# Optimization experiments

Hardware: AMD Instinct MI355X
Metric: run time of the kernel (lower is better)

Reference implementation:

```python
import jax, jax.numpy as jnp
import numpy as np

B, L, S, D, H = 32, 256, 64, 128, 4
DH = D // H
EPS = 1e-5


def _uniform(k, shape, scale):
    return jax.random.uniform(k, shape, jnp.float32, -scale, scale)


def setup_inputs() -> dict:
    key = jax.random.key(0)
    ks = jax.random.split(key, 12)
    sc = 1.0 / np.sqrt(D)
    return {
        "h_wq": jax.random.normal(ks[0], (B, L, D), jnp.float32),
        "h_all": jax.random.normal(ks[1], (B, L, S, D), jnp.float32),
        "station_id": jax.random.randint(ks[2], (B,), 0, S),
        "adj": jax.random.randint(ks[3], (S, S), 0, 2).astype(jnp.float32),
        "in_proj_w": _uniform(ks[4], (3 * D, D), sc),
        "in_proj_b": _uniform(ks[5], (3 * D,), sc),
        "out_w": _uniform(ks[6], (D, D), sc),
        "out_b": _uniform(ks[7], (D,), sc),
        "gate_w": _uniform(ks[8], (D, 2 * D), 1.0 / np.sqrt(2 * D)),
        "gate_b": _uniform(ks[9], (D,), 1.0 / np.sqrt(2 * D)),
        "ln_g": jnp.ones((D,), jnp.float32),
        "ln_b": jnp.zeros((D,), jnp.float32),
        "alpha": jnp.asarray(0.1, jnp.float32),
    }


def _allowed_mask(adj, station_id):
    # allowed[b, s] == True  <=> station s may attend as key for sample b
    sid = station_id.astype(jnp.int32)
    allowed = adj[sid] > 0.0                                  # [B, S]
    self_oh = jax.nn.one_hot(sid, adj.shape[0], dtype=bool)   # [B, S]
    allowed = allowed & ~self_oh                              # exclude self
    # fallback-to-all for rows with no neighbor (still excluding self)
    no_nb = ~jnp.any(allowed, axis=1, keepdims=True)
    allowed = jnp.where(no_nb, ~self_oh, allowed)
    # final safety: if STILL empty (S==1 edge case), allow self
    no_nb2 = ~jnp.any(allowed, axis=1, keepdims=True)
    allowed = allowed | (no_nb2 & self_oh)
    return allowed


def _forward(h_wq, h_all, station_id, adj, in_proj_w, in_proj_b,
             out_w, out_b, gate_w, gate_b, ln_g, ln_b, alpha):
    b, l, d = h_wq.shape
    s = h_all.shape[2]
    qw, kw, vw = jnp.split(in_proj_w, 3, axis=0)
    qb, kb, vb = jnp.split(in_proj_b, 3, axis=0)

    q = (h_wq @ qw.T + qb).reshape(b, l, H, DH)        # [B,L,H,DH]
    k = (h_all @ kw.T + kb).reshape(b, l, s, H, DH)    # [B,L,S,H,DH]
    v = (h_all @ vw.T + vb).reshape(b, l, s, H, DH)

    scores = jnp.einsum('blhd,blshd->blhs', q, k) / np.sqrt(DH)  # [B,L,H,S]
    allowed = _allowed_mask(adj, station_id)                     # [B,S]
    scores = jnp.where(allowed[:, None, None, :], scores, -jnp.inf)
    w = jax.nn.softmax(scores, axis=-1)

    ctx = jnp.einsum('blhs,blshd->blhd', w, v).reshape(b, l, d)
    ctx = ctx @ out_w.T + out_b                                  # out_proj

    g = jax.nn.sigmoid(jnp.concatenate([h_wq, ctx], axis=-1) @ gate_w.T + gate_b)
    y = h_wq + alpha * (g * ctx)                                 # dropout = eval mode

    mu = jnp.mean(y, axis=-1, keepdims=True)
    var = jnp.mean(jnp.square(y - mu), axis=-1, keepdims=True)
    return (y - mu) * jax.lax.rsqrt(var + EPS) * ln_g + ln_b


def reference(h_wq, h_all, station_id, adj, in_proj_w, in_proj_b,
              out_w, out_b, gate_w, gate_b, ln_g, ln_b, alpha):
    return _forward(h_wq, h_all, station_id, adj, in_proj_w, in_proj_b,
                    out_w, out_b, gate_w, gate_b, ln_g, ln_b, alpha)
```

## Files before the change

kernel.cpp:

```cpp
#include <hip/hip_runtime.h>
#include <math.h>

#define B_   32
#define L_   256
#define S_   64
#define D_   128
#define H_   4
#define DH_  32
#define NTOK (B_*L_)

#define QK_OFF   0
#define QK_BYTES ((size_t)NTOK*512*4)
#define CB_OFF   (QK_OFF + QK_BYTES)
#define CB_BYTES ((size_t)NTOK*4*4)
#define CTX_OFF  (CB_OFF + CB_BYTES)

__global__ __launch_bounds__(256) void qk_kernel(
        const float* __restrict__ h_wq,
        const float* __restrict__ in_proj_w, const float* __restrict__ in_proj_b,
        float* __restrict__ qk_out, float* __restrict__ cb_out) {
    __shared__ float x_lds[32*128];
    __shared__ float q_lds[32*128];
    const int t0 = blockIdx.x * 32;
    const int tid = threadIdx.x;

    {
        const float4* src = (const float4*)(h_wq + (size_t)t0*128);
        float4* dst = (float4*)x_lds;
        for (int e = tid; e < 32*32; e += 256) dst[e] = src[e];
    }
    __syncthreads();

    const int d = tid & 127, half = tid >> 7;
    const float* xb = x_lds + half*16*128;
    {
        float acc[16];
        const float qb = in_proj_b[d];
        #pragma unroll
        for (int t = 0; t < 16; ++t) acc[t] = qb;
        const float4* wrow = (const float4*)(in_proj_w + (size_t)d*128);
        for (int j4 = 0; j4 < 32; ++j4) {
            float4 w = wrow[j4];
            #pragma unroll
            for (int t = 0; t < 16; ++t) {
                float4 x = *(const float4*)(xb + t*128 + j4*4);
                acc[t] += w.x*x.x + w.y*x.y + w.z*x.z + w.w*x.w;
            }
        }
        #pragma unroll
        for (int t = 0; t < 16; ++t) q_lds[(half*16+t)*128 + d] = acc[t];
    }
    __syncthreads();

    const float scale = 0.17677669529663687f;
    const float* qbse = q_lds + half*16*128;
    #pragma unroll
    for (int h = 0; h < 4; ++h) {
        float acc[16];
        #pragma unroll
        for (int t = 0; t < 16; ++t) acc[t] = 0.f;
        for (int j = 0; j < 32; ++j) {
            float w = in_proj_w[(size_t)(128 + h*32 + j)*128 + d];
            #pragma unroll
            for (int t = 0; t < 16; ++t) acc[t] += w * qbse[t*128 + h*32 + j];
        }
        #pragma unroll
        for (int t = 0; t < 16; ++t)
            qk_out[(size_t)(t0 + half*16 + t)*512 + h*128 + d] = acc[t] * scale;
    }
    if (tid < 128) {
        int t = tid >> 2, h = tid & 3;
        float s = 0.f;
        for (int j = 0; j < 32; ++j)
            s += q_lds[t*128 + h*32 + j] * in_proj_b[128 + h*32 + j];
        cb_out[(t0 + t)*4 + h] = s * scale;
    }
}

__global__ __launch_bounds__(256) void attn_kernel(
        const float* __restrict__ h_all,
        const float* __restrict__ in_proj_w, const float* __restrict__ in_proj_b,
        const float* __restrict__ qk_buf, const float* __restrict__ cb_buf,
        const int* __restrict__ station_id, const float* __restrict__ adj,
        float* __restrict__ ctx_out) {
    __shared__ float qk_lds[4][4*132];
    __shared__ float sc[4][4*64];
    __shared__ float u_lds[4][4*132];
    __shared__ int   lst[64];
    __shared__ int   cnt_s;
    __shared__ float cb[4][4];

    const int t0  = blockIdx.x * 4;
    const int b   = t0 >> 8;
    const int tid = threadIdx.x;
    const int wv  = tid >> 6;
    const int lane = tid & 63;
    const int t = t0 + wv;

    if (tid < 64) {
        int sid = station_id[b];
        int s = tid;
        bool av = (adj[sid*S_ + s] > 0.0f) && (s != sid);
        unsigned long long m = __ballot(av);
        if (m == 0ull) { av = (s != sid); m = __ballot(av); }
        if (m == 0ull) { av = (s == sid); m = __ballot(av); }
        int idx = __popcll(m & ((1ull << s) - 1ull));
        if (av) lst[idx] = s;
        if (s == 0) cnt_s = __popcll(m);
    }

    {
        const float4* src = (const float4*)(qk_buf + (size_t)t*512);
        for (int e = lane; e < 128; e += 64) {
            int h = e >> 5, d4 = e & 31;
            *(float4*)&qk_lds[wv][h*132 + d4*4] = src[e];
        }
    }
    if (lane < 4) cb[wv][lane] = cb_buf[t*4 + lane];
    __syncthreads();

    const int cnt = cnt_s;
    const float* rowbase = h_all + (size_t)t * (S_*D_);

    for (int p = lane; p < 4*cnt; p += 64) {
        int h = p & 3, i = p >> 2;
        float acc = cb[wv][h];
        const float4* qr = (const float4*)(&qk_lds[wv][h*132]);
        const float4* rr = (const float4*)(rowbase + lst[i]*D_);
        #pragma unroll 8
        for (int j = 0; j < 32; ++j) {
            float4 a = qr[j], x = rr[j];
            acc += a.x*x.x + a.y*x.y + a.z*x.z + a.w*x.w;
        }
        sc[wv][h*64 + i] = acc;
    }

    {
        int j = lane & 31;
        for (int h = (lane >> 5); h < 4; h += 2) {
            float v0 = (j < cnt)      ? sc[wv][h*64 + j]      : -INFINITY;
            float v1 = (j + 32 < cnt) ? sc[wv][h*64 + j + 32] : -INFINITY;
            float m = fmaxf(v0, v1);
            for (int o = 16; o >= 1; o >>= 1) m = fmaxf(m, __shfl_xor(m, o, 32));
            float e0 = (j < cnt)      ? __expf(v0 - m) : 0.f;
            float e1 = (j + 32 < cnt) ? __expf(v1 - m) : 0.f;
            float ssum = e0 + e1;
            for (int o = 16; o >= 1; o >>= 1) ssum += __shfl_xor(ssum, o, 32);
            float inv = 1.0f / ssum;
            sc[wv][h*64 + j]      = e0 * inv;
            sc[wv][h*64 + j + 32] = e1 * inv;
        }
    }

    {
        float2 u0 = {0.f,0.f}, u1 = {0.f,0.f}, u2 = {0.f,0.f}, u3 = {0.f,0.f};
        #pragma unroll 4
        for (int i = 0; i < cnt; ++i) {
            float2 x = *(const float2*)(rowbase + lst[i]*D_ + 2*lane);
            float w0 = sc[wv][i], w1 = sc[wv][64+i], w2 = sc[wv][128+i], w3 = sc[wv][192+i];
            u0.x += w0*x.x; u0.y += w0*x.y;
            u1.x += w1*x.x; u1.y += w1*x.y;
            u2.x += w2*x.x; u2.y += w2*x.y;
            u3.x += w3*x.x; u3.y += w3*x.y;
        }
        *(float2*)&u_lds[wv][0*132 + 2*lane] = u0;
        *(float2*)&u_lds[wv][1*132 + 2*lane] = u1;
        *(float2*)&u_lds[wv][2*132 + 2*lane] = u2;
        *(float2*)&u_lds[wv][3*132 + 2*lane] = u3;
    }
    __syncthreads();

    if (tid < 128) {
        const int d = tid, h = d >> 5;
        const float4* vwrow = (const float4*)(in_proj_w + (size_t)(256 + d)*128);
        const float vb = in_proj_b[256 + d];
        float a0 = vb, a1 = vb, a2 = vb, a3 = vb;
        #pragma unroll 8
        for (int j4 = 0; j4 < 32; ++j4) {
            float4 w = vwrow[j4];
            float4 u0 = *(const float4*)(&u_lds[0][h*132 + j4*4]);
            float4 u1 = *(const float4*)(&u_lds[1][h*132 + j4*4]);
            float4 u2 = *(const float4*)(&u_lds[2][h*132 + j4*4]);
            float4 u3 = *(const float4*)(&u_lds[3][h*132 + j4*4]);
            a0 += w.x*u0.x + w.y*u0.y + w.z*u0.z + w.w*u0.w;
            a1 += w.x*u1.x + w.y*u1.y + w.z*u1.z + w.w*u1.w;
            a2 += w.x*u2.x + w.y*u2.y + w.z*u2.z + w.w*u2.w;
            a3 += w.x*u3.x + w.y*u3.y + w.z*u3.z + w.w*u3.w;
        }
        ctx_out[(size_t)(t0+0)*128 + d] = a0;
        ctx_out[(size_t)(t0+1)*128 + d] = a1;
        ctx_out[(size_t)(t0+2)*128 + d] = a2;
        ctx_out[(size_t)(t0+3)*128 + d] = a3;
    }
}

__global__ __launch_bounds__(256) void epi_kernel(
        const float* __restrict__ h_wq, const float* __restrict__ ctx_buf,
        const float* __restrict__ out_w, const float* __restrict__ out_b,
        const float* __restrict__ gate_w, const float* __restrict__ gate_b,
        const float* __restrict__ ln_g, const float* __restrict__ ln_b,
        const float* __restrict__ alpha, float* __restrict__ out) {
    __shared__ float c_tile[32*128];
    __shared__ float x_tile[32*128];
    __shared__ float o_tile[32*128];
    __shared__ float mu_s[32], rs_s[32];
    const int t0 = blockIdx.x * 32;
    const int tid = threadIdx.x;

    {
        const float4* cs = (const float4*)(ctx_buf + (size_t)t0*128);
        const float4* xs = (const float4*)(h_wq + (size_t)t0*128);
        float4* cd = (float4*)c_tile; float4* xd = (float4*)x_tile;
        for (int e = tid; e < 32*32; e += 256) { cd[e] = cs[e]; xd[e] = xs[e]; }
    }
    __syncthreads();

    const int d = tid & 127, half = tid >> 7;
    float o_acc[16];
    {
        const float ob = out_b[d];
        #pragma unroll
        for (int t = 0; t < 16; ++t) o_acc[t] = ob;
        const float4* wrow = (const float4*)(out_w + (size_t)d*128);
        const float* cbp = c_tile + half*16*128;
        for (int j4 = 0; j4 < 32; ++j4) {
            float4 w = wrow[j4];
            #pragma unroll
            for (int t = 0; t < 16; ++t) {
                float4 c = *(const float4*)(cbp + t*128 + j4*4);
                o_acc[t] += w.x*c.x + w.y*c.y + w.z*c.z + w.w*c.w;
            }
        }
        #pragma unroll
        for (int t = 0; t < 16; ++t) o_tile[(half*16+t)*128 + d] = o_acc[t];
    }
    __syncthreads();

    {
        float g_acc[16];
        const float gb = gate_b[d];
        #pragma unroll
        for (int t = 0; t < 16; ++t) g_acc[t] = gb;
        const float4* wrow = (const float4*)(gate_w + (size_t)d*256);
        const float* xb = x_tile + half*16*128;
        const float* obp = o_tile + half*16*128;
        for (int j4 = 0; j4 < 32; ++j4) {
            float4 w0 = wrow[j4];
            float4 w1 = wrow[32 + j4];
            #pragma unroll
            for (int t = 0; t < 16; ++t) {
                float4 x = *(const float4*)(xb  + t*128 + j4*4);
                float4 o = *(const float4*)(obp + t*128 + j4*4);
                g_acc[t] += w0.x*x.x + w0.y*x.y + w0.z*x.z + w0.w*x.w
                          + w1.x*o.x + w1.y*o.y + w1.z*o.z + w1.w*o.w;
            }
        }
        const float al = alpha[0];
        #pragma unroll
        for (int t = 0; t < 16; ++t) {
            float g = 1.0f / (1.0f + __expf(-g_acc[t]));
            float y = xb[t*128 + d] + al * g * o_acc[t];
            c_tile[(half*16+t)*128 + d] = y;
        }
    }
    __syncthreads();

    {
        int tt = tid >> 3, k = tid & 7;
        const float* yr = c_tile + tt*128;
        float s = 0.f;
        for (int dd = k; dd < 128; dd += 8) s += yr[dd];
        for (int o = 4; o >= 1; o >>= 1) s += __shfl_xor(s, o, 8);
        float mu = s * (1.0f/128.0f);
        float vs = 0.f;
        for (int dd = k; dd < 128; dd += 8) { float df = yr[dd] - mu; vs += df*df; }
        for (int o = 4; o >= 1; o >>= 1) vs += __shfl_xor(vs, o, 8);
        if (k == 0) { mu_s[tt] = mu; rs_s[tt] = rsqrtf(vs*(1.0f/128.0f) + 1e-5f); }
    }
    __syncthreads();

    for (int e = tid; e < 32*128; e += 256) {
        int tt = e >> 7, dd = e & 127;
        float y = c_tile[e];
        out[(size_t)t0*128 + e] = (y - mu_s[tt]) * rs_s[tt] * ln_g[dd] + ln_b[dd];
    }
}

extern "C" void kernel_launch(void* const* d_in, const int* in_sizes, int n_in,
                              void* d_out, int out_size, void* d_ws, size_t ws_size,
                              hipStream_t stream) {
    const float* h_wq       = (const float*)d_in[0];
    const float* h_all      = (const float*)d_in[1];
    const int*   station_id = (const int*)  d_in[2];
    const float* adj        = (const float*)d_in[3];
    const float* in_proj_w  = (const float*)d_in[4];
    const float* in_proj_b  = (const float*)d_in[5];
    const float* out_w      = (const float*)d_in[6];
    const float* out_b      = (const float*)d_in[7];
    const float* gate_w     = (const float*)d_in[8];
    const float* gate_b     = (const float*)d_in[9];
    const float* ln_g       = (const float*)d_in[10];
    const float* ln_b       = (const float*)d_in[11];
    const float* alpha      = (const float*)d_in[12];

    char* ws = (char*)d_ws;
    float* qk   = (float*)(ws + QK_OFF);
    float* cb   = (float*)(ws + CB_OFF);
    float* ctx  = (float*)(ws + CTX_OFF);
    float* out  = (float*)d_out;

    qk_kernel  <<<NTOK/32, 256, 0, stream>>>(h_wq, in_proj_w, in_proj_b, qk, cb);
    attn_kernel<<<NTOK/4, 256, 0, stream>>>(h_all, in_proj_w, in_proj_b, qk, cb,
                                            station_id, adj, ctx);
    epi_kernel <<<NTOK/32, 256, 0, stream>>>(h_wq, ctx, out_w, out_b, gate_w,
                                             gate_b, ln_g, ln_b, alpha, out);
}
```

Baseline: 448.0 us.

## Fuse score, softmax and value accumulation into single-pass online softmax

The attention kernel now computes per-station scores with wave-wide shuffle reductions and accumulates the weighted rows using an online softmax. Each gathered h_all row is read once instead of separately for scores and for the weighted sum. The q·Wk vectors and biases are kept in registers instead of LDS. In exchange it adds serial cross-lane shuffle reductions and extra exponentials per station, which may cost latency.

```diff
diff --git a/kernel.cpp b/kernel.cpp
--- a/kernel.cpp
+++ b/kernel.cpp
@@ -83,12 +83,9 @@
         const float* __restrict__ qk_buf, const float* __restrict__ cb_buf,
         const int* __restrict__ station_id, const float* __restrict__ adj,
         float* __restrict__ ctx_out) {
-    __shared__ float qk_lds[4][4*132];
-    __shared__ float sc[4][4*64];
     __shared__ float u_lds[4][4*132];
     __shared__ int   lst[64];
     __shared__ int   cnt_s;
-    __shared__ float cb[4][4];
 
     const int t0  = blockIdx.x * 4;
     const int b   = t0 >> 8;
@@ -109,60 +106,49 @@
         if (s == 0) cnt_s = __popcll(m);
     }
 
-    {
-        const float4* src = (const float4*)(qk_buf + (size_t)t*512);
-        for (int e = lane; e < 128; e += 64) {
-            int h = e >> 5, d4 = e & 31;
-            *(float4*)&qk_lds[wv][h*132 + d4*4] = src[e];
-        }
-    }
-    if (lane < 4) cb[wv][lane] = cb_buf[t*4 + lane];
-    __syncthreads();
-
+    const float* qkt = qk_buf + (size_t)t*512 + 2*lane;
+    const float2 qk0 = *(const float2*)(qkt);
+    const float2 qk1 = *(const float2*)(qkt + 128);
+    const float2 qk2 = *(const float2*)(qkt + 256);
+    const float2 qk3 = *(const float2*)(qkt + 384);
+    const float cb0 = cb_buf[t*4+0], cb1 = cb_buf[t*4+1];
+    const float cb2 = cb_buf[t*4+2], cb3 = cb_buf[t*4+3];
+
+    __syncthreads();
     const int cnt = cnt_s;
-    const float* rowbase = h_all + (size_t)t * (S_*D_);
-
-    for (int p = lane; p < 4*cnt; p += 64) {
-        int h = p & 3, i = p >> 2;
-        float acc = cb[wv][h];
-        const float4* qr = (const float4*)(&qk_lds[wv][h*132]);
-        const float4* rr = (const float4*)(rowbase + lst[i]*D_);
-        #pragma unroll 8
-        for (int j = 0; j < 32; ++j) {
-            float4 a = qr[j], x = rr[j];
-            acc += a.x*x.x + a.y*x.y + a.z*x.z + a.w*x.w;
-        }
-        sc[wv][h*64 + i] = acc;
-    }
-
-    {
-        int j = lane & 31;
-        for (int h = (lane >> 5); h < 4; h += 2) {
-            float v0 = (j < cnt)      ? sc[wv][h*64 + j]      : -INFINITY;
-            float v1 = (j + 32 < cnt) ? sc[wv][h*64 + j + 32] : -INFINITY;
-            float m = fmaxf(v0, v1);
-            for (int o = 16; o >= 1; o >>= 1) m = fmaxf(m, __shfl_xor(m, o, 32));
-            float e0 = (j < cnt)      ? __expf(v0 - m) : 0.f;
-            float e1 = (j + 32 < cnt) ? __expf(v1 - m) : 0.f;
-            float ssum = e0 + e1;
-            for (int o = 16; o >= 1; o >>= 1) ssum += __shfl_xor(ssum, o, 32);
-            float inv = 1.0f / ssum;
-            sc[wv][h*64 + j]      = e0 * inv;
-            sc[wv][h*64 + j + 32] = e1 * inv;
-        }
-    }
-
-    {
-        float2 u0 = {0.f,0.f}, u1 = {0.f,0.f}, u2 = {0.f,0.f}, u3 = {0.f,0.f};
-        #pragma unroll 4
-        for (int i = 0; i < cnt; ++i) {
-            float2 x = *(const float2*)(rowbase + lst[i]*D_ + 2*lane);
-            float w0 = sc[wv][i], w1 = sc[wv][64+i], w2 = sc[wv][128+i], w3 = sc[wv][192+i];
-            u0.x += w0*x.x; u0.y += w0*x.y;
-            u1.x += w1*x.x; u1.y += w1*x.y;
-            u2.x += w2*x.x; u2.y += w2*x.y;
-            u3.x += w3*x.x; u3.y += w3*x.y;
-        }
+    const float* rowbase = h_all + (size_t)t * (S_*D_) + 2*lane;
+
+    float m0 = -INFINITY, m1 = -INFINITY, m2 = -INFINITY, m3 = -INFINITY;
+    float l0 = 0.f, l1 = 0.f, l2 = 0.f, l3 = 0.f;
+    float2 u0 = {0.f,0.f}, u1 = {0.f,0.f}, u2 = {0.f,0.f}, u3 = {0.f,0.f};
+
+    for (int i = 0; i < cnt; ++i) {
+        float2 x = *(const float2*)(rowbase + lst[i]*D_);
+        float p0 = qk0.x*x.x + qk0.y*x.y;
+        float p1 = qk1.x*x.x + qk1.y*x.y;
+        float p2 = qk2.x*x.x + qk2.y*x.y;
+        float p3 = qk3.x*x.x + qk3.y*x.y;
+        #pragma unroll
+        for (int o = 32; o >= 1; o >>= 1) {
+            p0 += __shfl_xor(p0, o);
+            p1 += __shfl_xor(p1, o);
+            p2 += __shfl_xor(p2, o);
+            p3 += __shfl_xor(p3, o);
+        }
+        float s0 = p0 + cb0, s1 = p1 + cb1, s2 = p2 + cb2, s3 = p3 + cb3;
+        float n0 = fmaxf(m0, s0), r0 = __expf(m0 - n0), w0 = __expf(s0 - n0);
+        l0 = l0*r0 + w0; u0.x = u0.x*r0 + w0*x.x; u0.y = u0.y*r0 + w0*x.y; m0 = n0;
+        float n1 = fmaxf(m1, s1), r1 = __expf(m1 - n1), w1 = __expf(s1 - n1);
+        l1 = l1*r1 + w1; u1.x = u1.x*r1 + w1*x.x; u1.y = u1.y*r1 + w1*x.y; m1 = n1;
+        float n2 = fmaxf(m2, s2), r2 = __expf(m2 - n2), w2 = __expf(s2 - n2);
+        l2 = l2*r2 + w2; u2.x = u2.x*r2 + w2*x.x; u2.y = u2.y*r2 + w2*x.y; m2 = n2;
+        float n3 = fmaxf(m3, s3), r3 = __expf(m3 - n3), w3 = __expf(s3 - n3);
+        l3 = l3*r3 + w3; u3.x = u3.x*r3 + w3*x.x; u3.y = u3.y*r3 + w3*x.y; m3 = n3;
+    }
+    {
+        float i0 = 1.f/l0, i1 = 1.f/l1, i2 = 1.f/l2, i3 = 1.f/l3;
+        u0.x *= i0; u0.y *= i0;  u1.x *= i1; u1.y *= i1;
+        u2.x *= i2; u2.y *= i2;  u3.x *= i3; u3.y *= i3;
         *(float2*)&u_lds[wv][0*132 + 2*lane] = u0;
         *(float2*)&u_lds[wv][1*132 + 2*lane] = u1;
         *(float2*)&u_lds[wv][2*132 + 2*lane] = u2;
@@ -178,14 +164,14 @@
         #pragma unroll 8
         for (int j4 = 0; j4 < 32; ++j4) {
             float4 w = vwrow[j4];
-            float4 u0 = *(const float4*)(&u_lds[0][h*132 + j4*4]);
-            float4 u1 = *(const float4*)(&u_lds[1][h*132 + j4*4]);
-            float4 u2 = *(const float4*)(&u_lds[2][h*132 + j4*4]);
-            float4 u3 = *(const float4*)(&u_lds[3][h*132 + j4*4]);
-            a0 += w.x*u0.x + w.y*u0.y + w.z*u0.z + w.w*u0.w;
-            a1 += w.x*u1.x + w.y*u1.y + w.z*u1.z + w.w*u1.w;
-            a2 += w.x*u2.x + w.y*u2.y + w.z*u2.z + w.w*u2.w;
-            a3 += w.x*u3.x + w.y*u3.y + w.z*u3.z + w.w*u3.w;
+            float4 v0 = *(const float4*)(&u_lds[0][h*132 + j4*4]);
+            float4 v1 = *(const float4*)(&u_lds[1][h*132 + j4*4]);
+            float4 v2 = *(const float4*)(&u_lds[2][h*132 + j4*4]);
+            float4 v3 = *(const float4*)(&u_lds[3][h*132 + j4*4]);
+            a0 += w.x*v0.x + w.y*v0.y + w.z*v0.z + w.w*v0.w;
+            a1 += w.x*v1.x + w.y*v1.y + w.z*v1.z + w.w*v1.w;
+            a2 += w.x*v2.x + w.y*v2.y + w.z*v2.z + w.w*v2.w;
+            a3 += w.x*v3.x + w.y*v3.y + w.z*v3.z + w.w*v3.w;
         }
         ctx_out[(size_t)(t0+0)*128 + d] = a0;
         ctx_out[(size_t)(t0+1)*128 + d] = a1;
```

After: 471.3 us. 1.05x slower.
